# Kernel optimization log

Measured on AMD Instinct MI355X. Metric: run time of the kernel, lower is better.

## Reference

```python
import jax, jax.numpy as jnp
import numpy as np

B, S, D, H = 4, 2048, 512, 8
DH = D // H


def setup_inputs() -> dict:
    key = jax.random.key(0)
    ks = jax.random.split(key, 7)
    scale = 1.0 / np.sqrt(DH)  # mimic nn.Linear init magnitude
    return {
        "x": jax.random.normal(ks[0], (B, S, D), dtype=jnp.float32),
        "Wq": jax.random.normal(ks[1], (H, DH, DH), dtype=jnp.float32) * scale,
        "bq": jax.random.normal(ks[2], (H, DH), dtype=jnp.float32) * scale,
        "Wk": jax.random.normal(ks[3], (H, DH, DH), dtype=jnp.float32) * scale,
        "bk": jax.random.normal(ks[4], (H, DH), dtype=jnp.float32) * scale,
        "Wv": jax.random.normal(ks[5], (H, DH, DH), dtype=jnp.float32) * scale,
        "bv": jax.random.normal(ks[6], (H, DH), dtype=jnp.float32) * scale,
    }


def reference(x, Wq, bq, Wk, bk, Wv, bv):
    # x: [B, S, D] -> per-head slices [B, S, H, DH] (contiguous chunks, as in torch slicing)
    xh = x.reshape(B, S, H, DH)
    # nn.Linear: y = x @ W.T + b, per head. Wq[h] is [out, in].
    q = jnp.einsum("bshd,hed->bshe", xh, Wq) + bq  # [B, S, H, DH]
    k = jnp.einsum("bshd,hed->bshe", xh, Wk) + bk
    v = jnp.einsum("bshd,hed->bshe", xh, Wv) + bv
    scores = jnp.einsum("bshe,bthe->bhst", q, k) / jnp.sqrt(jnp.float32(DH))  # [B, H, S, S]
    attn = jax.nn.softmax(scores, axis=-1)
    out = jnp.einsum("bhst,bthe->bshe", attn, v)  # [B, S, H, DH]
    return out.reshape(B, S, D)  # hstack of head outputs == concat along feature dim
```

## Files before the change

kernel.cpp:

```cpp
#include <hip/hip_runtime.h>
#include <math.h>

#define B_ 4
#define S_ 2048
#define D_ 512
#define H_ 8
#define DH_ 64
#define BH_ (B_*H_)
#define SCALE 0.1803368801111243f

typedef __attribute__((ext_vector_type(4)))  float f32x4;
typedef __attribute__((ext_vector_type(16))) float f32x16;
typedef __attribute__((ext_vector_type(8)))  short bf16x8;

__device__ inline uint rnepk(float a, float b) {
    uint ua = __builtin_bit_cast(uint, a), ub = __builtin_bit_cast(uint, b);
    ua += 0x7FFFu + ((ua >> 16) & 1u);
    ub += 0x7FFFu + ((ub >> 16) & 1u);
    return (ua >> 16) | (ub & 0xFFFF0000u);
}
__device__ inline uint truncpk(float lo, float hi) {
    return __builtin_amdgcn_perm(__builtin_bit_cast(uint, hi),
                                 __builtin_bit_cast(uint, lo), 0x07060302u);
}
__device__ inline f32x16 zero16() {
    f32x16 z;
    #pragma unroll
    for (int i = 0; i < 16; ++i) z[i] = 0.f;
    return z;
}

__global__ __launch_bounds__(256, 2)
void qkv_mfma(const float* __restrict__ x,
              const float* __restrict__ Wq, const float* __restrict__ bq,
              const float* __restrict__ Wk, const float* __restrict__ bk,
              const float* __restrict__ Wv, const float* __restrict__ bv,
              ushort* __restrict__ Qb, ushort* __restrict__ Kb,
              ushort* __restrict__ Vtg)
{
    const int bh = blockIdx.x, b = bh >> 3, h = bh & 7;
    const int s0 = blockIdx.y * 128;
    const int tid = threadIdx.x;
    const int w = tid >> 6, lane = tid & 63, l31 = lane & 31, l5 = lane >> 5;

    __shared__ __align__(16) ushort xs[128 * 64];
    __shared__ __align__(16) ushort wl[3][64 * 64];
    __shared__ __align__(16) ushort bnc[4][2560];

    {
        const int row = tid >> 1, half = tid & 1;
        const float* xr = x + ((size_t)(b * S_ + s0 + row)) * D_ + h * DH_ + half * 32;
        ushort* dst = xs + row * 64;
        #pragma unroll
        for (int i = 0; i < 2; ++i) {
            float4 f0 = *(const float4*)(xr + i * 16);
            float4 f1 = *(const float4*)(xr + i * 16 + 4);
            float4 f2 = *(const float4*)(xr + i * 16 + 8);
            float4 f3 = *(const float4*)(xr + i * 16 + 12);
            uint4 c0, c1;
            c0.x = rnepk(f0.x, f0.y); c0.y = rnepk(f0.z, f0.w);
            c0.z = rnepk(f1.x, f1.y); c0.w = rnepk(f1.z, f1.w);
            c1.x = rnepk(f2.x, f2.y); c1.y = rnepk(f2.z, f2.w);
            c1.z = rnepk(f3.x, f3.y); c1.w = rnepk(f3.z, f3.w);
            const int ch0 = half * 4 + i * 2;
            *(uint4*)(dst + ((ch0 ^ (row & 7)) * 8)) = c0;
            *(uint4*)(dst + (((ch0 + 1) ^ (row & 7)) * 8)) = c1;
        }
    }
    {
        const float* Wm[3] = {Wq, Wk, Wv};
        #pragma unroll
        for (int it = 0; it < 6; ++it) {
            const int mat = it >> 1;
            const int e = (it & 1) * 32 + (tid >> 3), ch = tid & 7;
            const float* p = Wm[mat] + h * DH_ * DH_ + e * DH_ + ch * 8;
            float4 a = *(const float4*)(p);
            float4 c = *(const float4*)(p + 4);
            uint4 u;
            u.x = rnepk(a.x, a.y); u.y = rnepk(a.z, a.w);
            u.z = rnepk(c.x, c.y); u.w = rnepk(c.z, c.w);
            *(uint4*)(&wl[mat][e * 64 + ((ch ^ (e & 7)) * 8)]) = u;
        }
    }
    __syncthreads();

    const int srow = w * 32 + l31;
    bf16x8 xf[4];
    #pragma unroll
    for (int st = 0; st < 4; ++st)
        xf[st] = *(const bf16x8*)(xs + srow * 64 + (((st * 2 + l5) ^ (srow & 7)) * 8));

    ushort* mybnc = &bnc[w][0];

    #pragma unroll
    for (int mat = 0; mat < 2; ++mat) {
        const float* bias = mat ? bk : bq;
        f32x16 acc[2];
        #pragma unroll
        for (int et = 0; et < 2; ++et) {
            acc[et] = zero16();
            const int e = et * 32 + l31;
            #pragma unroll
            for (int st = 0; st < 4; ++st) {
                bf16x8 wf = *(const bf16x8*)(&wl[mat][e * 64 + (((st * 2 + l5) ^ (e & 7)) * 8)]);
                acc[et] = __builtin_amdgcn_mfma_f32_32x32x16_bf16(wf, xf[st], acc[et], 0, 0, 0);
            }
        }
        #pragma unroll
        for (int et = 0; et < 2; ++et)
            #pragma unroll
            for (int rg = 0; rg < 4; ++rg) {
                float4 b4 = *(const float4*)(bias + h * DH_ + et * 32 + rg * 8 + l5 * 4);
                float v0 = acc[et][rg * 4 + 0] + b4.x;
                float v1 = acc[et][rg * 4 + 1] + b4.y;
                float v2 = acc[et][rg * 4 + 2] + b4.z;
                float v3 = acc[et][rg * 4 + 3] + b4.w;
                if (mat == 0) { v0 *= SCALE; v1 *= SCALE; v2 *= SCALE; v3 *= SCALE; }
                uint2 pk;
                pk.x = rnepk(v0, v1); pk.y = rnepk(v2, v3);
                *(uint2*)(mybnc + l31 * 72 + et * 32 + rg * 8 + l5 * 4) = pk;
            }
        ushort* Og = mat ? Kb : Qb;
        #pragma unroll
        for (int i = 0; i < 4; ++i) {
            const int slot = lane + 64 * i;
            const int r = slot >> 3, c = slot & 7;
            uint4 v = *(const uint4*)(mybnc + r * 72 + c * 8);
            *(uint4*)(Og + ((size_t)(bh * S_ + s0 + w * 32 + r)) * DH_ + c * 8) = v;
        }
    }

    {
        f32x16 acc[2];
        #pragma unroll
        for (int et = 0; et < 2; ++et) {
            acc[et] = zero16();
            const int e = et * 32 + l31;
            #pragma unroll
            for (int st = 0; st < 4; ++st) {
                bf16x8 wf = *(const bf16x8*)(&wl[2][e * 64 + (((st * 2 + l5) ^ (e & 7)) * 8)]);
                acc[et] = __builtin_amdgcn_mfma_f32_32x32x16_bf16(xf[st], wf, acc[et], 0, 0, 0);
            }
        }
        const float bvv0 = bv[h * DH_ + l31], bvv1 = bv[h * DH_ + 32 + l31];
        #pragma unroll
        for (int et = 0; et < 2; ++et) {
            const float bb = et ? bvv1 : bvv0;
            #pragma unroll
            for (int rg = 0; rg < 4; ++rg) {
                float v0 = acc[et][rg * 4 + 0] + bb;
                float v1 = acc[et][rg * 4 + 1] + bb;
                float v2 = acc[et][rg * 4 + 2] + bb;
                float v3 = acc[et][rg * 4 + 3] + bb;
                uint2 pk;
                pk.x = rnepk(v0, v1); pk.y = rnepk(v2, v3);
                *(uint2*)(mybnc + (et * 32 + l31) * 40 + rg * 8 + l5 * 4) = pk;
            }
        }
        #pragma unroll
        for (int i = 0; i < 4; ++i) {
            const int slot = lane + 64 * i;
            const int r = slot >> 2, c = slot & 3;
            uint4 v = *(const uint4*)(mybnc + r * 40 + c * 8);
            *(uint4*)(Vtg + ((size_t)(bh * DH_ + r)) * S_ + s0 + w * 32 + c * 8) = v;
        }
    }
}

__global__ __launch_bounds__(256, 1)
void flash_mfma(const ushort* __restrict__ Qb, const ushort* __restrict__ Kb,
                const ushort* __restrict__ Vtg, float* __restrict__ out)
{
    const int blk = blockIdx.x;
    const int bh = blk & 31, qblk = blk >> 5;
    const int b = bh >> 3, h = bh & 7;
    const int tid = threadIdx.x;
    const int w = tid >> 6, lane = tid & 63, l31 = lane & 31, l5 = lane >> 5;

    __shared__ __align__(16) ushort lds_u[16384 + 4 * 64 * 72];
    ushort* Pw = lds_u + 16384 + w * (64 * 72);

    const int q0 = qblk * 256 + w * 64;
    bf16x8 qf[2][4];
    #pragma unroll
    for (int qt = 0; qt < 2; ++qt)
        #pragma unroll
        for (int st = 0; st < 4; ++st)
            qf[qt][st] = *(const bf16x8*)(Qb + ((size_t)(bh * S_ + q0 + qt * 32 + l31)) * DH_
                                          + st * 16 + l5 * 8);

    f32x16 O[2][2];
    #pragma unroll
    for (int i = 0; i < 2; ++i)
        #pragma unroll
        for (int j = 0; j < 2; ++j) O[i][j] = zero16();
    float lsum[2] = {0.f, 0.f};

    const ushort* kg = Kb + (size_t)bh * S_ * DH_;
    const ushort* vg = Vtg + (size_t)bh * DH_ * S_;
    const int sr0 = tid >> 3, sc0 = tid & 7;
    const int sr1 = (tid + 256) >> 3, sc1 = tid & 7;

    uint4 kv0, kv1, vv0, vv1;
    kv0 = *(const uint4*)(kg + (size_t)sr0 * DH_ + sc0 * 8);
    kv1 = *(const uint4*)(kg + (size_t)sr1 * DH_ + sc1 * 8);
    vv0 = *(const uint4*)(vg + (size_t)sr0 * S_ + sc0 * 8);
    vv1 = *(const uint4*)(vg + (size_t)sr1 * S_ + sc1 * 8);
    *(uint4*)(lds_u + sr0 * 64 + ((sc0 ^ (sr0 & 7)) * 8)) = kv0;
    *(uint4*)(lds_u + sr1 * 64 + ((sc1 ^ (sr1 & 7)) * 8)) = kv1;
    *(uint4*)(lds_u + 8192 + sr0 * 64 + ((sc0 ^ (sr0 & 7)) * 8)) = vv0;
    *(uint4*)(lds_u + 8192 + sr1 * 64 + ((sc1 ^ (sr1 & 7)) * 8)) = vv1;

    for (int kt = 0; kt < 32; ++kt) {
        __syncthreads();
        const int cur = kt & 1, nxt = cur ^ 1;
        if (kt < 31) {
            const size_t ko = (size_t)(kt + 1) * 64 * DH_;
            const int vo = (kt + 1) * 64;
            kv0 = *(const uint4*)(kg + ko + (size_t)sr0 * DH_ + sc0 * 8);
            kv1 = *(const uint4*)(kg + ko + (size_t)sr1 * DH_ + sc1 * 8);
            vv0 = *(const uint4*)(vg + (size_t)sr0 * S_ + vo + sc0 * 8);
            vv1 = *(const uint4*)(vg + (size_t)sr1 * S_ + vo + sc1 * 8);
        }
        const ushort* ksb = lds_u + cur * 4096;
        const ushort* vsb = lds_u + 8192 + cur * 4096;

        #pragma unroll
        for (int kt32 = 0; kt32 < 2; ++kt32) {
            const int key = kt32 * 32 + l31;
            bf16x8 kf[4];
            #pragma unroll
            for (int st = 0; st < 4; ++st)
                kf[st] = *(const bf16x8*)(ksb + key * 64 + (((st * 2 + l5) ^ (key & 7)) * 8));
            #pragma unroll
            for (int qt = 0; qt < 2; ++qt) {
                f32x16 sc = zero16();
                #pragma unroll
                for (int st = 0; st < 4; ++st)
                    sc = __builtin_amdgcn_mfma_f32_32x32x16_bf16(kf[st], qf[qt][st], sc, 0, 0, 0);
                float ls = 0.f;
                #pragma unroll
                for (int rg = 0; rg < 4; ++rg) {
                    float p0 = __builtin_amdgcn_exp2f(sc[rg * 4 + 0]);
                    float p1 = __builtin_amdgcn_exp2f(sc[rg * 4 + 1]);
                    float p2 = __builtin_amdgcn_exp2f(sc[rg * 4 + 2]);
                    float p3 = __builtin_amdgcn_exp2f(sc[rg * 4 + 3]);
                    ls += (p0 + p1) + (p2 + p3);
                    uint2 pk;
                    pk.x = truncpk(p0, p1); pk.y = truncpk(p2, p3);
                    *(uint2*)(Pw + (qt * 32 + l31) * 72 + kt32 * 32 + rg * 8 + l5 * 4) = pk;
                }
                lsum[qt] += ls;
            }
        }

        bf16x8 pf[2][4];
        #pragma unroll
        for (int qt = 0; qt < 2; ++qt)
            #pragma unroll
            for (int st = 0; st < 4; ++st)
                pf[qt][st] = *(const bf16x8*)(Pw + (qt * 32 + l31) * 72 + st * 16 + l5 * 8);
        #pragma unroll
        for (int dht = 0; dht < 2; ++dht) {
            const int dh = dht * 32 + l31;
            bf16x8 vf[4];
            #pragma unroll
            for (int st = 0; st < 4; ++st)
                vf[st] = *(const bf16x8*)(vsb + dh * 64 + (((st * 2 + l5) ^ (dh & 7)) * 8));
            #pragma unroll
            for (int qt = 0; qt < 2; ++qt)
                #pragma unroll
                for (int st = 0; st < 4; ++st)
                    O[dht][qt] = __builtin_amdgcn_mfma_f32_32x32x16_bf16(vf[st], pf[qt][st],
                                                                          O[dht][qt], 0, 0, 0);
        }

        if (kt < 31) {
            ushort* kn = lds_u + nxt * 4096;
            ushort* vn = lds_u + 8192 + nxt * 4096;
            *(uint4*)(kn + sr0 * 64 + ((sc0 ^ (sr0 & 7)) * 8)) = kv0;
            *(uint4*)(kn + sr1 * 64 + ((sc1 ^ (sr1 & 7)) * 8)) = kv1;
            *(uint4*)(vn + sr0 * 64 + ((sc0 ^ (sr0 & 7)) * 8)) = vv0;
            *(uint4*)(vn + sr1 * 64 + ((sc1 ^ (sr1 & 7)) * 8)) = vv1;
        }
    }

    #pragma unroll
    for (int qt = 0; qt < 2; ++qt) {
        float l = lsum[qt] + __shfl_xor(lsum[qt], 32);
        lsum[qt] = 1.0f / l;
    }
    #pragma unroll
    for (int dht = 0; dht < 2; ++dht)
        #pragma unroll
        for (int qt = 0; qt < 2; ++qt)
            #pragma unroll
            for (int i = 0; i < 16; ++i) O[dht][qt][i] *= lsum[qt];

    __syncthreads();
    float* ob = (float*)lds_u + w * (64 * 68);
    #pragma unroll
    for (int dht = 0; dht < 2; ++dht)
        #pragma unroll
        for (int qt = 0; qt < 2; ++qt)
            #pragma unroll
            for (int rg = 0; rg < 4; ++rg) {
                f32x4 v4;
                v4[0] = O[dht][qt][rg * 4 + 0];
                v4[1] = O[dht][qt][rg * 4 + 1];
                v4[2] = O[dht][qt][rg * 4 + 2];
                v4[3] = O[dht][qt][rg * 4 + 3];
                *(f32x4*)(ob + (qt * 32 + l31) * 68 + dht * 32 + rg * 8 + l5 * 4) = v4;
            }
    #pragma unroll
    for (int i = 0; i < 16; ++i) {
        const int slot = lane + 64 * i;
        const int r = slot >> 4, c = slot & 15;
        f32x4 v = *(const f32x4*)(ob + r * 68 + c * 4);
        *(f32x4*)(out + ((size_t)(b * S_ + q0 + r)) * D_ + h * DH_ + c * 4) = v;
    }
}

extern "C" void kernel_launch(void* const* d_in, const int* in_sizes, int n_in,
                              void* d_out, int out_size, void* d_ws, size_t ws_size,
                              hipStream_t stream) {
    const float* x  = (const float*)d_in[0];
    const float* Wq = (const float*)d_in[1];
    const float* bq = (const float*)d_in[2];
    const float* Wk = (const float*)d_in[3];
    const float* bk = (const float*)d_in[4];
    const float* Wv = (const float*)d_in[5];
    const float* bv = (const float*)d_in[6];
    float* outp = (float*)d_out;

    ushort* Qb  = (ushort*)d_ws;
    ushort* Kb  = Qb + (size_t)BH_ * S_ * DH_;
    ushort* Vtg = Kb + (size_t)BH_ * S_ * DH_;

    qkv_mfma<<<dim3(BH_, S_ / 128), 256, 0, stream>>>(x, Wq, bq, Wk, bk, Wv, bv,
                                                      Qb, Kb, Vtg);
    flash_mfma<<<dim3(BH_ * 8), 256, 0, stream>>>(Qb, Kb, Vtg, outp);
}
```

Baseline: 143.3 us.

## Halve per-block query tile, single-buffer K/V, and double flash grid size

The flash kernel now has each wave handle 32 query rows instead of 64, so a block covers 128 queries and the grid grows from 256 to 512 blocks. K/V staging in LDS drops from double to single buffering, with an extra barrier before the next tile is written. Launch bounds now allow two blocks per CU. The aim is to fill more CUs and hide latency through occupancy, at the cost of reading K/V twice as often overall and a second barrier per iteration.

After: 133.3 us. -7.0%, faster.

```diff
diff --git a/kernel.cpp b/kernel.cpp
--- a/kernel.cpp
+++ b/kernel.cpp
@@ -12,6 +12,7 @@
 typedef __attribute__((ext_vector_type(4)))  float f32x4;
 typedef __attribute__((ext_vector_type(16))) float f32x16;
 typedef __attribute__((ext_vector_type(8)))  short bf16x8;
+typedef __attribute__((ext_vector_type(4)))  uint  u32x4;
 
 __device__ inline uint rnepk(float a, float b) {
     uint ua = __builtin_bit_cast(uint, a), ub = __builtin_bit_cast(uint, b);
@@ -148,12 +149,9 @@
             const float bb = et ? bvv1 : bvv0;
             #pragma unroll
             for (int rg = 0; rg < 4; ++rg) {
-                float v0 = acc[et][rg * 4 + 0] + bb;
-                float v1 = acc[et][rg * 4 + 1] + bb;
-                float v2 = acc[et][rg * 4 + 2] + bb;
-                float v3 = acc[et][rg * 4 + 3] + bb;
                 uint2 pk;
-                pk.x = rnepk(v0, v1); pk.y = rnepk(v2, v3);
+                pk.x = rnepk(acc[et][rg * 4 + 0] + bb, acc[et][rg * 4 + 1] + bb);
+                pk.y = rnepk(acc[et][rg * 4 + 2] + bb, acc[et][rg * 4 + 3] + bb);
                 *(uint2*)(mybnc + (et * 32 + l31) * 40 + rg * 8 + l5 * 4) = pk;
             }
         }
@@ -167,7 +165,7 @@
     }
 }
 
-__global__ __launch_bounds__(256, 1)
+__global__ __launch_bounds__(256, 2)
 void flash_mfma(const ushort* __restrict__ Qb, const ushort* __restrict__ Kb,
                 const ushort* __restrict__ Vtg, float* __restrict__ out)
 {
@@ -177,143 +175,122 @@
     const int tid = threadIdx.x;
     const int w = tid >> 6, lane = tid & 63, l31 = lane & 31, l5 = lane >> 5;
 
-    __shared__ __align__(16) ushort lds_u[16384 + 4 * 64 * 72];
-    ushort* Pw = lds_u + 16384 + w * (64 * 72);
-
-    const int q0 = qblk * 256 + w * 64;
-    bf16x8 qf[2][4];
-    #pragma unroll
-    for (int qt = 0; qt < 2; ++qt)
-        #pragma unroll
-        for (int st = 0; st < 4; ++st)
-            qf[qt][st] = *(const bf16x8*)(Qb + ((size_t)(bh * S_ + q0 + qt * 32 + l31)) * DH_
-                                          + st * 16 + l5 * 8);
-
-    f32x16 O[2][2];
-    #pragma unroll
-    for (int i = 0; i < 2; ++i)
-        #pragma unroll
-        for (int j = 0; j < 2; ++j) O[i][j] = zero16();
-    float lsum[2] = {0.f, 0.f};
+    __shared__ __align__(16) ushort lds_u[17408];
+    ushort* Ks = lds_u;
+    ushort* Vs = lds_u + 4096;
+    ushort* Pw = lds_u + 8192 + w * (32 * 68);
+
+    const int q0 = qblk * 128 + w * 32;
+    bf16x8 qf[4];
+    #pragma unroll
+    for (int st = 0; st < 4; ++st)
+        qf[st] = *(const bf16x8*)(Qb + ((size_t)(bh * S_ + q0 + l31)) * DH_
+                                  + st * 16 + l5 * 8);
+
+    f32x16 O[2];
+    O[0] = zero16(); O[1] = zero16();
+    float lsum = 0.f;
 
     const ushort* kg = Kb + (size_t)bh * S_ * DH_;
     const ushort* vg = Vtg + (size_t)bh * DH_ * S_;
-    const int sr0 = tid >> 3, sc0 = tid & 7;
-    const int sr1 = (tid + 256) >> 3, sc1 = tid & 7;
-
-    uint4 kv0, kv1, vv0, vv1;
-    kv0 = *(const uint4*)(kg + (size_t)sr0 * DH_ + sc0 * 8);
-    kv1 = *(const uint4*)(kg + (size_t)sr1 * DH_ + sc1 * 8);
-    vv0 = *(const uint4*)(vg + (size_t)sr0 * S_ + sc0 * 8);
-    vv1 = *(const uint4*)(vg + (size_t)sr1 * S_ + sc1 * 8);
-    *(uint4*)(lds_u + sr0 * 64 + ((sc0 ^ (sr0 & 7)) * 8)) = kv0;
-    *(uint4*)(lds_u + sr1 * 64 + ((sc1 ^ (sr1 & 7)) * 8)) = kv1;
-    *(uint4*)(lds_u + 8192 + sr0 * 64 + ((sc0 ^ (sr0 & 7)) * 8)) = vv0;
-    *(uint4*)(lds_u + 8192 + sr1 * 64 + ((sc1 ^ (sr1 & 7)) * 8)) = vv1;
+    const int sr0 = tid >> 3, sc = tid & 7, sr1 = sr0 + 32;
+
+    uint4 kv0 = *(const uint4*)(kg + (size_t)sr0 * DH_ + sc * 8);
+    uint4 kv1 = *(const uint4*)(kg + (size_t)sr1 * DH_ + sc * 8);
+    uint4 vv0 = *(const uint4*)(vg + (size_t)sr0 * S_ + sc * 8);
+    uint4 vv1 = *(const uint4*)(vg + (size_t)sr1 * S_ + sc * 8);
+    *(uint4*)(Ks + sr0 * 64 + ((sc ^ (sr0 & 7)) * 8)) = kv0;
+    *(uint4*)(Ks + sr1 * 64 + ((sc ^ (sr1 & 7)) * 8)) = kv1;
+    *(uint4*)(Vs + sr0 * 64 + ((sc ^ (sr0 & 7)) * 8)) = vv0;
+    *(uint4*)(Vs + sr1 * 64 + ((sc ^ (sr1 & 7)) * 8)) = vv1;
 
     for (int kt = 0; kt < 32; ++kt) {
         __syncthreads();
-        const int cur = kt & 1, nxt = cur ^ 1;
         if (kt < 31) {
             const size_t ko = (size_t)(kt + 1) * 64 * DH_;
             const int vo = (kt + 1) * 64;
-            kv0 = *(const uint4*)(kg + ko + (size_t)sr0 * DH_ + sc0 * 8);
-            kv1 = *(const uint4*)(kg + ko + (size_t)sr1 * DH_ + sc1 * 8);
-            vv0 = *(const uint4*)(vg + (size_t)sr0 * S_ + vo + sc0 * 8);
-            vv1 = *(const uint4*)(vg + (size_t)sr1 * S_ + vo + sc1 * 8);
-        }
-        const ushort* ksb = lds_u + cur * 4096;
-        const ushort* vsb = lds_u + 8192 + cur * 4096;
-
-        #pragma unroll
-        for (int kt32 = 0; kt32 < 2; ++kt32) {
-            const int key = kt32 * 32 + l31;
+            kv0 = *(const uint4*)(kg + ko + (size_t)sr0 * DH_ + sc * 8);
+            kv1 = *(const uint4*)(kg + ko + (size_t)sr1 * DH_ + sc * 8);
+            vv0 = *(const uint4*)(vg + (size_t)sr0 * S_ + vo + sc * 8);
+            vv1 = *(const uint4*)(vg + (size_t)sr1 * S_ + vo + sc * 8);
+        }
+
+        #pragma unroll
+        for (int g = 0; g < 2; ++g) {
+            const int key = g * 32 + l31;
             bf16x8 kf[4];
             #pragma unroll
             for (int st = 0; st < 4; ++st)
-                kf[st] = *(const bf16x8*)(ksb + key * 64 + (((st * 2 + l5) ^ (key & 7)) * 8));
-            #pragma unroll
-            for (int qt = 0; qt < 2; ++qt) {
-                f32x16 sc = zero16();
-                #pragma unroll
-                for (int st = 0; st < 4; ++st)
-                    sc = __builtin_amdgcn_mfma_f32_32x32x16_bf16(kf[st], qf[qt][st], sc, 0, 0, 0);
-                float ls = 0.f;
-                #pragma unroll
-                for (int rg = 0; rg < 4; ++rg) {
-                    float p0 = __builtin_amdgcn_exp2f(sc[rg * 4 + 0]);
-                    float p1 = __builtin_amdgcn_exp2f(sc[rg * 4 + 1]);
-                    float p2 = __builtin_amdgcn_exp2f(sc[rg * 4 + 2]);
-                    float p3 = __builtin_amdgcn_exp2f(sc[rg * 4 + 3]);
-                    ls += (p0 + p1) + (p2 + p3);
-                    uint2 pk;
-                    pk.x = truncpk(p0, p1); pk.y = truncpk(p2, p3);
-                    *(uint2*)(Pw + (qt * 32 + l31) * 72 + kt32 * 32 + rg * 8 + l5 * 4) = pk;
-                }
-                lsum[qt] += ls;
-            }
-        }
-
-        bf16x8 pf[2][4];
-        #pragma unroll
-        for (int qt = 0; qt < 2; ++qt)
+                kf[st] = *(const bf16x8*)(Ks + key * 64 + (((st * 2 + l5) ^ (key & 7)) * 8));
+            f32x16 sc_ = zero16();
             #pragma unroll
             for (int st = 0; st < 4; ++st)
-                pf[qt][st] = *(const bf16x8*)(Pw + (qt * 32 + l31) * 72 + st * 16 + l5 * 8);
+                sc_ = __builtin_amdgcn_mfma_f32_32x32x16_bf16(kf[st], qf[st], sc_, 0, 0, 0);
+            #pragma unroll
+            for (int rg = 0; rg < 4; ++rg) {
+                float p0 = __builtin_amdgcn_exp2f(sc_[rg * 4 + 0]);
+                float p1 = __builtin_amdgcn_exp2f(sc_[rg * 4 + 1]);
+                float p2 = __builtin_amdgcn_exp2f(sc_[rg * 4 + 2]);
+                float p3 = __builtin_amdgcn_exp2f(sc_[rg * 4 + 3]);
+                lsum += (p0 + p1) + (p2 + p3);
+                uint2 pk;
+                pk.x = truncpk(p0, p1); pk.y = truncpk(p2, p3);
+                *(uint2*)(Pw + l31 * 68 + g * 32 + rg * 8 + l5 * 4) = pk;
+            }
+        }
+
+        bf16x8 pf[4];
+        #pragma unroll
+        for (int st = 0; st < 4; ++st) {
+            const ushort* pp = Pw + l31 * 68 + st * 16 + l5 * 8;
+            uint2 lo = *(const uint2*)(pp);
+            uint2 hi = *(const uint2*)(pp + 4);
+            u32x4 t; t.x = lo.x; t.y = lo.y; t.z = hi.x; t.w = hi.y;
+            pf[st] = __builtin_bit_cast(bf16x8, t);
+        }
         #pragma unroll
         for (int dht = 0; dht < 2; ++dht) {
             const int dh = dht * 32 + l31;
             bf16x8 vf[4];
             #pragma unroll
             for (int st = 0; st < 4; ++st)
-                vf[st] = *(const bf16x8*)(vsb + dh * 64 + (((st * 2 + l5) ^ (dh & 7)) * 8));
-            #pragma unroll
-            for (int qt = 0; qt < 2; ++qt)
-                #pragma unroll
-                for (int st = 0; st < 4; ++st)
-                    O[dht][qt] = __builtin_amdgcn_mfma_f32_32x32x16_bf16(vf[st], pf[qt][st],
-                                                                          O[dht][qt], 0, 0, 0);
-        }
-
+                vf[st] = *(const bf16x8*)(Vs + dh * 64 + (((st * 2 + l5) ^ (dh & 7)) * 8));
+            #pragma unroll
+            for (int st = 0; st < 4; ++st)
+                O[dht] = __builtin_amdgcn_mfma_f32_32x32x16_bf16(vf[st], pf[st], O[dht], 0, 0, 0);
+        }
+
+        __syncthreads();
         if (kt < 31) {
-            ushort* kn = lds_u + nxt * 4096;
-            ushort* vn = lds_u + 8192 + nxt * 4096;
-            *(uint4*)(kn + sr0 * 64 + ((sc0 ^ (sr0 & 7)) * 8)) = kv0;
-            *(uint4*)(kn + sr1 * 64 + ((sc1 ^ (sr1 & 7)) * 8)) = kv1;
-            *(uint4*)(vn + sr0 * 64 + ((sc0 ^ (sr0 & 7)) * 8)) = vv0;
-            *(uint4*)(vn + sr1 * 64 + ((sc1 ^ (sr1 & 7)) * 8)) = vv1;
-        }
-    }
-
-    #pragma unroll
-    for (int qt = 0; qt < 2; ++qt) {
-        float l = lsum[qt] + __shfl_xor(lsum[qt], 32);
-        lsum[qt] = 1.0f / l;
-    }
+            *(uint4*)(Ks + sr0 * 64 + ((sc ^ (sr0 & 7)) * 8)) = kv0;
+            *(uint4*)(Ks + sr1 * 64 + ((sc ^ (sr1 & 7)) * 8)) = kv1;
+            *(uint4*)(Vs + sr0 * 64 + ((sc ^ (sr0 & 7)) * 8)) = vv0;
+            *(uint4*)(Vs + sr1 * 64 + ((sc ^ (sr1 & 7)) * 8)) = vv1;
+        }
+    }
+
+    lsum += __shfl_xor(lsum, 32);
+    const float linv = 1.0f / lsum;
     #pragma unroll
     for (int dht = 0; dht < 2; ++dht)
         #pragma unroll
-        for (int qt = 0; qt < 2; ++qt)
-            #pragma unroll
-            for (int i = 0; i < 16; ++i) O[dht][qt][i] *= lsum[qt];
+        for (int i = 0; i < 16; ++i) O[dht][i] *= linv;
 
     __syncthreads();
-    float* ob = (float*)lds_u + w * (64 * 68);
+    float* ob = (float*)lds_u + w * (32 * 68);
     #pragma unroll
     for (int dht = 0; dht < 2; ++dht)
         #pragma unroll
-        for (int qt = 0; qt < 2; ++qt)
-            #pragma unroll
-            for (int rg = 0; rg < 4; ++rg) {
-                f32x4 v4;
-                v4[0] = O[dht][qt][rg * 4 + 0];
-                v4[1] = O[dht][qt][rg * 4 + 1];
-                v4[2] = O[dht][qt][rg * 4 + 2];
-                v4[3] = O[dht][qt][rg * 4 + 3];
-                *(f32x4*)(ob + (qt * 32 + l31) * 68 + dht * 32 + rg * 8 + l5 * 4) = v4;
-            }
-    #pragma unroll
-    for (int i = 0; i < 16; ++i) {
+        for (int rg = 0; rg < 4; ++rg) {
+            f32x4 v4;
+            v4[0] = O[dht][rg * 4 + 0];
+            v4[1] = O[dht][rg * 4 + 1];
+            v4[2] = O[dht][rg * 4 + 2];
+            v4[3] = O[dht][rg * 4 + 3];
+            *(f32x4*)(ob + l31 * 68 + dht * 32 + rg * 8 + l5 * 4) = v4;
+        }
+    #pragma unroll
+    for (int i = 0; i < 8; ++i) {
         const int slot = lane + 64 * i;
         const int r = slot >> 4, c = slot & 15;
         f32x4 v = *(const f32x4*)(ob + r * 68 + c * 4);
@@ -339,5 +316,5 @@
 
     qkv_mfma<<<dim3(BH_, S_ / 128), 256, 0, stream>>>(x, Wq, bq, Wk, bk, Wv, bv,
                                                       Qb, Kb, Vtg);
-    flash_mfma<<<dim3(BH_ * 8), 256, 0, stream>>>(Qb, Kb, Vtg, outp);
-}
+    flash_mfma<<<dim3(32 * 16), 256, 0, stream>>>(Qb, Kb, Vtg, outp);
+}
```
